# Performance work log

Measured on AMD Instinct MI355X. Metric: run time of the kernel, lower is better.

Reference implementation:

```python
import jax, jax.numpy as jnp
import numpy as np

ETA = 3.0
KCAP = 96
POS_W = 1.2
LAMBDA_CD = 1.0
LAMBDA_P0 = 1.0
STRIDES = (8.0, 16.0, 32.0)


def _level_terms(pred_reg, pred_obj, pred_cls, gt, stride):
    """Vectorized per-level version of the triple python loop.
    pred_reg: [B,6,H,W], pred_obj/pred_cls: [B,1,H,W], gt: [B,Ng,3,2].
    Returns partial sums (reg, obj, cls, pos_count, neg_count)."""
    B, _, H, W = pred_obj.shape
    HW = H * W
    Ng = gt.shape[1]
    ys = (jnp.arange(H, dtype=jnp.float32) + 0.5) * stride
    xs = (jnp.arange(W, dtype=jnp.float32) + 0.5) * stride
    yy, xx = jnp.meshgrid(ys, xs, indexing='ij')
    px = xx.reshape(-1)  # [HW]
    py = yy.reshape(-1)
    P = px[None, None, :]  # [1,1,HW]
    Q = py[None, None, :]
    # triangle vertices, each [B,Ng,1] for broadcasting against HW
    Ax, Ay = gt[:, :, 0, 0:1], gt[:, :, 0, 1:2]
    Bx, By = gt[:, :, 1, 0:1], gt[:, :, 1, 1:2]
    Cx, Cy = gt[:, :, 2, 0:1], gt[:, :, 2, 1:2]

    def sgn(x1, y1, x2, y2, x3, y3):
        return (x1 - x3) * (y2 - y3) - (x2 - x3) * (y1 - y3)

    d1 = sgn(P, Q, Ax, Ay, Bx, By)
    d2 = sgn(P, Q, Bx, By, Cx, Cy)
    d3 = sgn(P, Q, Cx, Cy, Ax, Ay)
    has_neg = (d1 < 0) | (d2 < 0) | (d3 < 0)
    has_pos = (d1 > 0) | (d2 > 0) | (d3 > 0)
    inside = ~(has_neg & has_pos)  # [B,Ng,HW]

    def segd(x1, y1, x2, y2):
        vx, vy = x2 - x1, y2 - y1
        wx, wy = P - x1, Q - y1
        t = jnp.clip((wx * vx + wy * vy) / (vx * vx + vy * vy + 1e-9), 0.0, 1.0)
        dx = P - (x1 + t * vx)
        dy = Q - (y1 + t * vy)
        return jnp.sqrt(dx * dx + dy * dy + 1e-12)

    dist = jnp.minimum(segd(Ax, Ay, Bx, By),
                       jnp.minimum(segd(Bx, By, Cx, Cy), segd(Cx, Cy, Ax, Ay)))
    pos = inside | (dist <= ETA)  # [B,Ng,HW]

    # top-k cap: keep the KCAP positives with smallest boundary distance
    dmask = jnp.where(pos, dist, jnp.inf)
    negd, idx = jax.lax.top_k(-dmask, KCAP)  # [B,Ng,K]
    keep = jnp.isfinite(negd)                # finite <=> was a positive
    bi = jnp.arange(B)[:, None, None]
    gi = jnp.arange(Ng)[None, :, None]
    capped = jnp.zeros((B, Ng, HW), dtype=bool).at[bi, gi, idx].set(keep)
    m = capped.astype(jnp.float32)
    pos_count = m.sum()

    # objectness BCE-with-logits (pos_weight) over the whole map
    obj_t = capped.any(axis=1).astype(jnp.float32)  # [B,HW]
    x = pred_obj.reshape(B, HW)
    obj_loss = (POS_W * obj_t * jax.nn.softplus(-x)
                + (1.0 - obj_t) * jax.nn.softplus(x)).sum()
    neg_count = jnp.float32(B * HW) - obj_t.sum()

    pred_off = pred_reg.transpose(0, 2, 3, 1).reshape(B, HW, 3, 2)
    centers = jnp.stack([px, py], axis=-1)  # [HW,2]
    gt_off = (gt[:, :, None] - centers[None, None, :, None]) / stride  # [B,Ng,HW,3,2]
    p0 = ((pred_off[:, None, :, 0] - gt_off[:, :, :, 0]) ** 2).sum(-1)  # [B,Ng,HW]
    pp = pred_off[:, None, :, 1:, :]  # [B,1,HW,2,2]
    gg = gt_off[:, :, :, 1:, :]       # [B,Ng,HW,2,2]
    d = jnp.sqrt(((pp[..., :, None, :] - gg[..., None, :, :]) ** 2).sum(-1))  # [B,Ng,HW,2,2]
    cd = d.min(-1).sum(-1) + d.min(-2).sum(-1)  # [B,Ng,HW]
    reg = (m * (LAMBDA_P0 * p0 + LAMBDA_CD * cd)).sum()

    # class BCE on positives only, target = 1
    cls = (m * jax.nn.softplus(-pred_cls.reshape(B, 1, HW))).sum()
    return reg, obj_loss, cls, pos_count, neg_count


def setup_inputs() -> dict:
    key = jax.random.key(0)
    ks = jax.random.split(key, 10)
    B, Ng = 16, 32
    shapes = [(128, 128), (64, 64), (32, 32)]
    inp = {}
    i = 0
    for l, (H, W) in enumerate(shapes):
        inp[f'pred_reg{l}'] = jax.random.normal(ks[i], (B, 6, H, W), dtype=jnp.float32); i += 1
        inp[f'pred_obj{l}'] = jax.random.normal(ks[i], (B, 1, H, W), dtype=jnp.float32); i += 1
        inp[f'pred_cls{l}'] = jax.random.normal(ks[i], (B, 1, H, W), dtype=jnp.float32); i += 1
    inp['gt'] = jax.random.uniform(ks[9], (B, Ng, 3, 2), dtype=jnp.float32) * 1024.0
    return inp


def reference(pred_reg0, pred_obj0, pred_cls0,
              pred_reg1, pred_obj1, pred_cls1,
              pred_reg2, pred_obj2, pred_cls2, gt):
    levels = [(pred_reg0, pred_obj0, pred_cls0),
              (pred_reg1, pred_obj1, pred_cls1),
              (pred_reg2, pred_obj2, pred_cls2)]
    reg = obj = cls = pc = nc = jnp.float32(0.0)
    for (pr, po, pcls), s in zip(levels, STRIDES):
        r, o, c, p, n = _level_terms(pr, po, pcls, gt, s)
        reg += r; obj += o; cls += c; pc += p; nc += n
    pos_eps = jnp.maximum(pc, 1.0)
    total = (reg / pos_eps
             + obj / (pos_eps + jnp.maximum(nc, 1.0))
             + cls / pos_eps)
    return total
```

## Files before the change

### kernel.cpp

```cpp
#include <hip/hip_runtime.h>

#define KCAP 96u
#define CAP 6144
#define PBLK 512
#define NTOT 344064
#define NPAIR 1536
#define CELLS_PB 224

__device__ __forceinline__ float softplus_f(float x) {
    return fmaxf(x, 0.0f) + log1pf(expf(-fabsf(x)));
}

__device__ __forceinline__ void tri_pos_dist(
    float px, float py,
    float ax, float ay, float bx, float by, float cx, float cy,
    bool& pos, float& dist)
{
#pragma clang fp contract(off)
    float d1 = (px - bx) * (ay - by) - (ax - bx) * (py - by);
    float d2 = (px - cx) * (by - cy) - (bx - cx) * (py - cy);
    float d3 = (px - ax) * (cy - ay) - (cx - ax) * (py - ay);
    bool has_neg = (d1 < 0.f) | (d2 < 0.f) | (d3 < 0.f);
    bool has_pos = (d1 > 0.f) | (d2 > 0.f) | (d3 > 0.f);
    bool inside = !(has_neg && has_pos);

    float dAB, dBC, dCA;
    {
        float vx = bx - ax, vy = by - ay, wx = px - ax, wy = py - ay;
        float t = (wx*vx + wy*vy) / (vx*vx + vy*vy + 1e-9f);
        t = fminf(fmaxf(t, 0.0f), 1.0f);
        float dx = px - (ax + t*vx), dy = py - (ay + t*vy);
        dAB = sqrtf(dx*dx + dy*dy + 1e-12f);
    }
    {
        float vx = cx - bx, vy = cy - by, wx = px - bx, wy = py - by;
        float t = (wx*vx + wy*vy) / (vx*vx + vy*vy + 1e-9f);
        t = fminf(fmaxf(t, 0.0f), 1.0f);
        float dx = px - (bx + t*vx), dy = py - (by + t*vy);
        dBC = sqrtf(dx*dx + dy*dy + 1e-12f);
    }
    {
        float vx = ax - cx, vy = ay - cy, wx = px - cx, wy = py - cy;
        float t = (wx*vx + wy*vy) / (vx*vx + vy*vy + 1e-9f);
        t = fminf(fmaxf(t, 0.0f), 1.0f);
        float dx = px - (cx + t*vx), dy = py - (cy + t*vy);
        dCA = sqrtf(dx*dx + dy*dy + 1e-12f);
    }
    dist = fminf(dAB, fminf(dBC, dCA));
    pos = inside || (dist <= 3.0f);
}

__global__ void zero_kernel(unsigned* __restrict__ p, int n) {
    int i = blockIdx.x * 256 + threadIdx.x;
    if (i < n) p[i] = 0u;
}

__global__ __launch_bounds__(PBLK) void pair_kernel(
    const float* __restrict__ gt,
    const float* __restrict__ reg0, const float* __restrict__ cls0, const float* __restrict__ o0,
    const float* __restrict__ reg1, const float* __restrict__ cls1, const float* __restrict__ o1,
    const float* __restrict__ reg2, const float* __restrict__ cls2, const float* __restrict__ o2,
    unsigned* __restrict__ objbits,
    double* __restrict__ p_reg, double* __restrict__ p_cls,
    double* __restrict__ p_obj, unsigned* __restrict__ p_tc,
    unsigned* __restrict__ p_pos)
{
    const int bid = blockIdx.x;
    const int tid = threadIdx.x;
    const int lane = tid & 63;

    const int level = bid >> 9;
    const int pair = bid & 511;
    const int b = pair >> 5;

    int W, HW, shift, objbase;
    float stride;
    const float* pr; const float* pcl; const float* po;
    if (level == 0)      { W = 128; HW = 16384; shift = 7; stride = 8.0f;  objbase = 0;     pr = reg0; pcl = cls0; po = o0; }
    else if (level == 1) { W = 64;  HW = 4096;  shift = 6; stride = 16.0f; objbase = 8192;  pr = reg1; pcl = cls1; po = o1; }
    else                 { W = 32;  HW = 1024;  shift = 5; stride = 32.0f; objbase = 10240; pr = reg2; pcl = cls2; po = o2; }
    const int wmask = W - 1;

    double objAcc = 0.0;
    if (tid < CELLS_PB) {
        int idx = bid * CELLS_PB + tid;
        const float* o; int li;
        if (idx < 262144)      { o = o0; li = idx; }
        else if (idx < 327680) { o = o1; li = idx - 262144; }
        else                   { o = o2; li = idx - 327680; }
        objAcc = (double)softplus_f(o[li]);
    }

    const float* gp = gt + pair * 6;
    const float ax = gp[0], ay = gp[1];
    const float bx = gp[2], by = gp[3];
    const float cx = gp[4], cy = gp[5];

    const float inv = 1.0f / stride;
    float minx = fminf(ax, fminf(bx, cx)), maxx = fmaxf(ax, fmaxf(bx, cx));
    float miny = fminf(ay, fminf(by, cy)), maxy = fmaxf(ay, fmaxf(by, cy));
    int wlo = max(0,     (int)floorf((minx - 3.0f) * inv - 0.5f) - 1);
    int whi = min(W - 1, (int)ceilf ((maxx + 3.0f) * inv - 0.5f) + 1);
    int hlo = max(0,     (int)floorf((miny - 3.0f) * inv - 0.5f) - 1);
    int hhi = min(W - 1, (int)ceilf ((maxy + 3.0f) * inv - 0.5f) + 1);
    const int ncols = max(0, whi - wlo + 1);
    const int nb = (hhi - hlo + 1 > 0) ? (hhi - hlo + 1) * ncols : 0;
    const int nbR = (nb + PBLK - 1) & ~(PBLK - 1);
    const unsigned long long dmul =
        (ncols > 0) ? ((1ull << 40) / (unsigned)ncols + 1ull) : 0ull;

    __shared__ unsigned hist[2048];
    __shared__ unsigned chunk[256];
    __shared__ unsigned chunk4[64];
    __shared__ unsigned s_bits[CAP];
    __shared__ unsigned short s_hw[CAP];
    __shared__ unsigned s_cnt, s_T, s_k, s_tiecnt;
    __shared__ double red_reg[8], red_cls[8], red_obj[8];
    __shared__ unsigned red_tc[8], red_pos[8];
    unsigned* tie_hw = hist;

    if (tid == 0) { s_cnt = 0u; s_tiecnt = 0u; }
    for (int j = tid; j < 2048; j += PBLK) hist[j] = 0u;
    __syncthreads();

    auto kth_scan = [&](unsigned kk) {
        __syncthreads();
        if (tid < 256) {
            unsigned s = 0; int base = tid * 8;
            #pragma unroll
            for (int j = 0; j < 8; ++j) s += hist[base + j];
            chunk[tid] = s;
        }
        __syncthreads();
        if (tid < 64) {
            int b4 = tid * 4;
            chunk4[tid] = chunk[b4] + chunk[b4+1] + chunk[b4+2] + chunk[b4+3];
        }
        __syncthreads();
        if (tid == 0) {
            unsigned cum = 0; int t4 = 0;
            while (cum + chunk4[t4] < kk) { cum += chunk4[t4]; ++t4; }
            int t = t4 * 4;
            while (cum + chunk[t] < kk) { cum += chunk[t]; ++t; }
            int bb = t * 8;
            while (cum + hist[bb] < kk) { cum += hist[bb]; ++bb; }
            s_T = (unsigned)bb;
            s_k = kk - cum;
        }
        __syncthreads();
    };

    for (int i = tid; i < nbR; i += PBLK) {
        bool pos = false; unsigned bits = 0u; int hw = 0;
        if (i < nb) {
            int q = (int)(((unsigned long long)(unsigned)i * dmul) >> 40);
            int w = wlo + (i - q * ncols);
            int h = hlo + q;
            hw = (h << shift) | w;
            float px = (w + 0.5f) * stride;
            float py = (h + 0.5f) * stride;
            float dist;
            tri_pos_dist(px, py, ax, ay, bx, by, cx, cy, pos, dist);
            if (pos) { bits = __float_as_uint(dist); atomicAdd(&hist[bits >> 21], 1u); }
        }
        unsigned long long m = __ballot(pos);
        if (m) {
            int leader = __ffsll(m) - 1;
            unsigned base = 0u;
            if (lane == leader) base = atomicAdd(&s_cnt, (unsigned)__popcll(m));
            base = __shfl(base, leader);
            if (pos) {
                unsigned slot = base + (unsigned)__popcll(m & ((1ull << lane) - 1ull));
                if (slot < CAP) { s_bits[slot] = bits; s_hw[slot] = (unsigned short)hw; }
            }
        }
    }
    __syncthreads();

    const unsigned total = s_cnt;
    const bool fullsel = (total <= KCAP);
    unsigned n = min(total, (unsigned)CAP);
    unsigned kth_bits = 0u, tie_need = 0u;
    bool radix_fb = false;

    if (!fullsel) {
        kth_scan(KCAP);
        const unsigned T = s_T, kk1 = s_k;

        if (total > CAP) {
            if (tid == 0) s_cnt = 0u;
            __syncthreads();
            for (int i = tid; i < nbR; i += PBLK) {
                bool keep = false; unsigned bits = 0u; int hw = 0;
                if (i < nb) {
                    int q = (int)(((unsigned long long)(unsigned)i * dmul) >> 40);
                    int w = wlo + (i - q * ncols);
                    int h = hlo + q;
                    hw = (h << shift) | w;
                    float px = (w + 0.5f) * stride;
                    float py = (h + 0.5f) * stride;
                    bool pos; float dist;
                    tri_pos_dist(px, py, ax, ay, bx, by, cx, cy, pos, dist);
                    if (pos) {
                        bits = __float_as_uint(dist);
                        keep = ((bits >> 21) <= T);
                    }
                }
                unsigned long long m = __ballot(keep);
                if (m) {
                    int leader = __ffsll(m) - 1;
                    unsigned base = 0u;
                    if (lane == leader) base = atomicAdd(&s_cnt, (unsigned)__popcll(m));
                    base = __shfl(base, leader);
                    if (keep) {
                        unsigned slot = base + (unsigned)__popcll(m & ((1ull << lane) - 1ull));
                        if (slot < CAP) { s_bits[slot] = bits; s_hw[slot] = (unsigned short)hw; }
                    }
                }
            }
            __syncthreads();
            n = s_cnt;
            if (n > CAP) { radix_fb = true; }
        }

        if (!radix_fb) {
            __syncthreads();
            for (int j = tid; j < 2048; j += PBLK) hist[j] = 0u;
            __syncthreads();
            for (unsigned i = tid; i < n; i += PBLK) {
                unsigned bi = s_bits[i];
                if ((bi >> 21) == T) atomicAdd(&hist[(bi >> 10) & 0x7FFu], 1u);
            }
            kth_scan(kk1);
            unsigned prefix = (T << 11) | s_T;
            unsigned kk2 = s_k;
            __syncthreads();
            for (int j = tid; j < 2048; j += PBLK) hist[j] = 0u;
            __syncthreads();
            for (unsigned i = tid; i < n; i += PBLK) {
                unsigned bi = s_bits[i];
                if ((bi >> 10) == prefix) atomicAdd(&hist[bi & 0x3FFu], 1u);
            }
            kth_scan(kk2);
            kth_bits = (prefix << 10) | s_T;
            tie_need = s_k;
        }
    }

    double regAcc = 0.0, clsAcc = 0.0;
    unsigned tcAcc = 0u, posAcc = 0u;

    auto contribute = [&](int hw) {
        int h = hw >> shift, w = hw & wmask;
        float px = (w + 0.5f) * stride;
        float py = (h + 0.5f) * stride;
        const float* base = pr + (size_t)b * 6 * HW + hw;
        float p0x = base[0],          p0y = base[HW];
        float p1x = base[2 * HW],     p1y = base[3 * HW];
        float p2x = base[4 * HW],     p2y = base[5 * HW];
        float g0x = (ax - px) * inv,  g0y = (ay - py) * inv;
        float g1x = (bx - px) * inv,  g1y = (by - py) * inv;
        float g2x = (cx - px) * inv,  g2y = (cy - py) * inv;
        float dx0 = p0x - g0x, dy0 = p0y - g0y;
        float p0t = dx0 * dx0 + dy0 * dy0;
        float e11x = p1x - g1x, e11y = p1y - g1y;
        float e12x = p1x - g2x, e12y = p1y - g2y;
        float e21x = p2x - g1x, e21y = p2y - g1y;
        float e22x = p2x - g2x, e22y = p2y - g2y;
        float d11 = sqrtf(e11x * e11x + e11y * e11y);
        float d12 = sqrtf(e12x * e12x + e12y * e12y);
        float d21 = sqrtf(e21x * e21x + e21y * e21y);
        float d22 = sqrtf(e22x * e22x + e22y * e22y);
        float cd = fminf(d11, d12) + fminf(d21, d22) + fminf(d11, d21) + fminf(d12, d22);
        regAcc += (double)(p0t + cd);
        clsAcc += (double)softplus_f(-pcl[(size_t)b * HW + hw]);
        posAcc += 1u;

        unsigned bi = (unsigned)(b * HW + hw);
        unsigned bit = 1u << (bi & 31u);
        unsigned old = atomicOr(&objbits[objbase + (bi >> 5)], bit);
        if (!(old & bit)) {
            float x = po[(size_t)b * HW + hw];
            objAcc += (double)(1.2f * softplus_f(-x)) - (double)softplus_f(x);
            tcAcc += 1u;
        }
    };

    if (fullsel) {
        for (unsigned i = tid; i < n; i += PBLK) contribute((int)s_hw[i]);
    } else if (!radix_fb) {
        for (unsigned i = tid; i < n; i += PBLK) {
            unsigned bi = s_bits[i];
            if (bi < kth_bits) {
                contribute((int)s_hw[i]);
            } else if (bi == kth_bits) {
                unsigned t = atomicAdd(&s_tiecnt, 1u);
                if (t < 2048u) tie_hw[t] = s_hw[i];
            }
        }
        __syncthreads();
        unsigned tn = min(s_tiecnt, 2048u);
        for (unsigned i = tid; i < tn; i += PBLK) {
            unsigned hwv = tie_hw[i], rank = 0;
            for (unsigned j = 0; j < tn; ++j) rank += (tie_hw[j] < hwv) ? 1u : 0u;
            if (rank < tie_need) contribute((int)hwv);
        }
    } else {
        unsigned prefix = s_T;
        for (int p = 1; p < 3; ++p) {
            unsigned kk = s_k;
            __syncthreads();
            for (int j = tid; j < 2048; j += PBLK) hist[j] = 0u;
            __syncthreads();
            for (int i = tid; i < nb; i += PBLK) {
                int q = (int)(((unsigned long long)(unsigned)i * dmul) >> 40);
                int w = wlo + (i - q * ncols);
                int h = hlo + q;
                float px = (w + 0.5f) * stride;
                float py = (h + 0.5f) * stride;
                bool pos; float dist;
                tri_pos_dist(px, py, ax, ay, bx, by, cx, cy, pos, dist);
                if (!pos) continue;
                unsigned bits = __float_as_uint(dist);
                unsigned bin;
                if (p == 1) { if ((bits >> 21) != prefix) continue; bin = (bits >> 10) & 0x7FFu; }
                else        { if ((bits >> 10) != prefix) continue; bin = bits & 0x3FFu; }
                atomicAdd(&hist[bin], 1u);
            }
            kth_scan(kk);
            prefix = (p == 1) ? ((prefix << 11) | s_T) : ((prefix << 10) | s_T);
        }
        const unsigned kth = prefix, need = s_k;
        for (int i = tid; i < nb; i += PBLK) {
            int q = (int)(((unsigned long long)(unsigned)i * dmul) >> 40);
            int w = wlo + (i - q * ncols);
            int h = hlo + q;
            int hw = (h << shift) | w;
            float px = (w + 0.5f) * stride;
            float py = (h + 0.5f) * stride;
            bool pos; float dist;
            tri_pos_dist(px, py, ax, ay, bx, by, cx, cy, pos, dist);
            if (!pos) continue;
            unsigned bits = __float_as_uint(dist);
            if (bits < kth) {
                contribute(hw);
            } else if (bits == kth) {
                unsigned t = atomicAdd(&s_tiecnt, 1u);
                if (t < 2048u) tie_hw[t] = (unsigned)hw;
            }
        }
        __syncthreads();
        unsigned tn = min(s_tiecnt, 2048u);
        for (unsigned i = tid; i < tn; i += PBLK) {
            unsigned hwv = tie_hw[i], rank = 0;
            for (unsigned j = 0; j < tn; ++j) rank += (tie_hw[j] < hwv) ? 1u : 0u;
            if (rank < need) contribute((int)hwv);
        }
    }

    for (int off = 32; off > 0; off >>= 1) {
        regAcc += __shfl_down(regAcc, off);
        clsAcc += __shfl_down(clsAcc, off);
        objAcc += __shfl_down(objAcc, off);
        tcAcc  += __shfl_down(tcAcc, off);
        posAcc += __shfl_down(posAcc, off);
    }
    int wave = tid >> 6;
    if (lane == 0) {
        red_reg[wave] = regAcc; red_cls[wave] = clsAcc; red_obj[wave] = objAcc;
        red_tc[wave] = tcAcc; red_pos[wave] = posAcc;
    }
    __syncthreads();
    if (tid == 0) {
        double rs = 0.0, cs = 0.0, os = 0.0; unsigned ts = 0u, ps = 0u;
        #pragma unroll
        for (int i = 0; i < 8; ++i) {
            rs += red_reg[i]; cs += red_cls[i]; os += red_obj[i];
            ts += red_tc[i]; ps += red_pos[i];
        }
        p_reg[bid] = rs;
        p_cls[bid] = cs;
        p_obj[bid] = os;
        p_tc[bid]  = ts;
        p_pos[bid] = ps;
    }
}

__global__ __launch_bounds__(1024) void finalize_kernel(
    const double* __restrict__ p_reg, const double* __restrict__ p_cls,
    const double* __restrict__ p_obj, const unsigned* __restrict__ p_tc,
    const unsigned* __restrict__ p_pos,
    float* __restrict__ out)
{
    const int tid = threadIdx.x;
    double reg = 0.0, cls = 0.0, obj = 0.0;
    unsigned pc = 0u, tc = 0u;
    for (int i = tid; i < NPAIR; i += 1024) {
        reg += p_reg[i]; cls += p_cls[i]; obj += p_obj[i];
        tc += p_tc[i]; pc += p_pos[i];
    }
    for (int off = 32; off > 0; off >>= 1) {
        reg += __shfl_down(reg, off);
        cls += __shfl_down(cls, off);
        obj += __shfl_down(obj, off);
        pc  += __shfl_down(pc, off);
        tc  += __shfl_down(tc, off);
    }
    __shared__ double rr[16], rc[16], ro[16];
    __shared__ unsigned rp[16], rn[16];
    int wave = tid >> 6, lane = tid & 63;
    if (lane == 0) { rr[wave] = reg; rc[wave] = cls; ro[wave] = obj; rp[wave] = pc; rn[wave] = tc; }
    __syncthreads();
    if (tid == 0) {
        double sreg = 0, scls = 0, sobj = 0; unsigned spc = 0, stc = 0;
        #pragma unroll
        for (int i = 0; i < 16; ++i) {
            sreg += rr[i]; scls += rc[i]; sobj += ro[i]; spc += rp[i]; stc += rn[i];
        }
        double nc = (double)NTOT - (double)stc;
        double pos_eps = fmax((double)spc, 1.0);
        double den = pos_eps + fmax(nc, 1.0);
        out[0] = (float)(sreg / pos_eps + sobj / den + scls / pos_eps);
    }
}

extern "C" void kernel_launch(void* const* d_in, const int* in_sizes, int n_in,
                              void* d_out, int out_size, void* d_ws, size_t ws_size,
                              hipStream_t stream)
{
    (void)in_sizes; (void)n_in; (void)out_size; (void)ws_size;
    const float* reg0 = (const float*)d_in[0];
    const float* obj0 = (const float*)d_in[1];
    const float* cls0 = (const float*)d_in[2];
    const float* reg1 = (const float*)d_in[3];
    const float* obj1 = (const float*)d_in[4];
    const float* cls1 = (const float*)d_in[5];
    const float* reg2 = (const float*)d_in[6];
    const float* obj2 = (const float*)d_in[7];
    const float* cls2 = (const float*)d_in[8];
    const float* gt   = (const float*)d_in[9];

    char* ws = (char*)d_ws;
    unsigned* objbits = (unsigned*)ws;
    double*   p_reg   = (double*)(ws + 43008);
    double*   p_cls   = (double*)(ws + 55296);
    double*   p_obj   = (double*)(ws + 67584);
    unsigned* p_tc    = (unsigned*)(ws + 79872);
    unsigned* p_pos   = (unsigned*)(ws + 86016);

    zero_kernel<<<42, 256, 0, stream>>>(objbits, 10752);
    pair_kernel<<<NPAIR, PBLK, 0, stream>>>(gt,
                                            reg0, cls0, obj0,
                                            reg1, cls1, obj1,
                                            reg2, cls2, obj2,
                                            objbits,
                                            p_reg, p_cls, p_obj, p_tc, p_pos);
    finalize_kernel<<<1, 1024, 0, stream>>>(p_reg, p_cls, p_obj, p_tc, p_pos,
                                            (float*)d_out);
}
```

Baseline: 145.1 us.

## Schedule pair blocks largest-bbox-first via on-device bitonic sort

```diff
diff --git a/kernel.cpp b/kernel.cpp
--- a/kernel.cpp
+++ b/kernel.cpp
@@ -50,9 +50,64 @@
     pos = inside || (dist <= 3.0f);
 }
 
-__global__ void zero_kernel(unsigned* __restrict__ p, int n) {
-    int i = blockIdx.x * 256 + threadIdx.x;
-    if (i < n) p[i] = 0u;
+__device__ __forceinline__ unsigned bbox_cells(const float* gp, int level) {
+    int W; float stride;
+    if (level == 0)      { W = 128; stride = 8.0f;  }
+    else if (level == 1) { W = 64;  stride = 16.0f; }
+    else                 { W = 32;  stride = 32.0f; }
+    const float inv = 1.0f / stride;
+    float ax = gp[0], ay = gp[1], bx = gp[2], by = gp[3], cx = gp[4], cy = gp[5];
+    float minx = fminf(ax, fminf(bx, cx)), maxx = fmaxf(ax, fmaxf(bx, cx));
+    float miny = fminf(ay, fminf(by, cy)), maxy = fmaxf(ay, fmaxf(by, cy));
+    int wlo = max(0,     (int)floorf((minx - 3.0f) * inv - 0.5f) - 1);
+    int whi = min(W - 1, (int)ceilf ((maxx + 3.0f) * inv - 0.5f) + 1);
+    int hlo = max(0,     (int)floorf((miny - 3.0f) * inv - 0.5f) - 1);
+    int hhi = min(W - 1, (int)ceilf ((maxy + 3.0f) * inv - 0.5f) + 1);
+    int ncols = max(0, whi - wlo + 1);
+    int nrows = hhi - hlo + 1;
+    return (nrows > 0) ? (unsigned)(nrows * ncols) : 0u;
+}
+
+__global__ __launch_bounds__(1024) void schedule_kernel(
+    const float* __restrict__ gt,
+    unsigned* __restrict__ objbits,
+    unsigned short* __restrict__ perm)
+{
+    const int t = threadIdx.x;
+    for (int i = t; i < 10752; i += 1024) objbits[i] = 0u;
+
+    __shared__ unsigned d[2048];
+    #pragma unroll
+    for (int s = 0; s < 2; ++s) {
+        int i = t + s * 1024;
+        unsigned packed = 0u;
+        if (i < NPAIR) {
+            unsigned nb = bbox_cells(gt + (i & 511) * 6, i >> 9);
+            packed = (nb << 11) | (unsigned)i;
+        }
+        d[i] = packed;
+    }
+    __syncthreads();
+    for (unsigned k = 2; k <= 2048u; k <<= 1) {
+        for (unsigned j = k >> 1; j > 0; j >>= 1) {
+            #pragma unroll
+            for (int s = 0; s < 2; ++s) {
+                int i = t + s * 1024;
+                int ixj = i ^ (int)j;
+                if (ixj > i) {
+                    unsigned a = d[i], b = d[ixj];
+                    bool desc = ((i & k) == 0);
+                    if (desc ? (a < b) : (a > b)) { d[i] = b; d[ixj] = a; }
+                }
+            }
+            __syncthreads();
+        }
+    }
+    #pragma unroll
+    for (int s = 0; s < 2; ++s) {
+        int i = t + s * 1024;
+        if (i < NPAIR) perm[i] = (unsigned short)(d[i] & 0x7FFu);
+    }
 }
 
 __global__ __launch_bounds__(PBLK) void pair_kernel(
@@ -60,17 +115,18 @@
     const float* __restrict__ reg0, const float* __restrict__ cls0, const float* __restrict__ o0,
     const float* __restrict__ reg1, const float* __restrict__ cls1, const float* __restrict__ o1,
     const float* __restrict__ reg2, const float* __restrict__ cls2, const float* __restrict__ o2,
+    const unsigned short* __restrict__ perm,
     unsigned* __restrict__ objbits,
     double* __restrict__ p_reg, double* __restrict__ p_cls,
     double* __restrict__ p_obj, unsigned* __restrict__ p_tc,
     unsigned* __restrict__ p_pos)
 {
-    const int bid = blockIdx.x;
+    const int pid = (int)perm[blockIdx.x];
     const int tid = threadIdx.x;
     const int lane = tid & 63;
 
-    const int level = bid >> 9;
-    const int pair = bid & 511;
+    const int level = pid >> 9;
+    const int pair = pid & 511;
     const int b = pair >> 5;
 
     int W, HW, shift, objbase;
@@ -83,7 +139,7 @@
 
     double objAcc = 0.0;
     if (tid < CELLS_PB) {
-        int idx = bid * CELLS_PB + tid;
+        int idx = pid * CELLS_PB + tid;
         const float* o; int li;
         if (idx < 262144)      { o = o0; li = idx; }
         else if (idx < 327680) { o = o1; li = idx - 262144; }
@@ -378,11 +434,11 @@
             rs += red_reg[i]; cs += red_cls[i]; os += red_obj[i];
             ts += red_tc[i]; ps += red_pos[i];
         }
-        p_reg[bid] = rs;
-        p_cls[bid] = cs;
-        p_obj[bid] = os;
-        p_tc[bid]  = ts;
-        p_pos[bid] = ps;
+        p_reg[pid] = rs;
+        p_cls[pid] = cs;
+        p_obj[pid] = os;
+        p_tc[pid]  = ts;
+        p_pos[pid] = ps;
     }
 }
 
@@ -441,19 +497,20 @@
     const float* gt   = (const float*)d_in[9];
 
     char* ws = (char*)d_ws;
-    unsigned* objbits = (unsigned*)ws;
-    double*   p_reg   = (double*)(ws + 43008);
-    double*   p_cls   = (double*)(ws + 55296);
-    double*   p_obj   = (double*)(ws + 67584);
-    unsigned* p_tc    = (unsigned*)(ws + 79872);
-    unsigned* p_pos   = (unsigned*)(ws + 86016);
-
-    zero_kernel<<<42, 256, 0, stream>>>(objbits, 10752);
+    unsigned*       objbits = (unsigned*)ws;
+    double*         p_reg   = (double*)(ws + 43008);
+    double*         p_cls   = (double*)(ws + 55296);
+    double*         p_obj   = (double*)(ws + 67584);
+    unsigned*       p_tc    = (unsigned*)(ws + 79872);
+    unsigned*       p_pos   = (unsigned*)(ws + 86016);
+    unsigned short* perm    = (unsigned short*)(ws + 92160);
+
+    schedule_kernel<<<1, 1024, 0, stream>>>(gt, objbits, perm);
     pair_kernel<<<NPAIR, PBLK, 0, stream>>>(gt,
                                             reg0, cls0, obj0,
                                             reg1, cls1, obj1,
                                             reg2, cls2, obj2,
-                                            objbits,
+                                            perm, objbits,
                                             p_reg, p_cls, p_obj, p_tc, p_pos);
     finalize_kernel<<<1, 1024, 0, stream>>>(p_reg, p_cls, p_obj, p_tc, p_pos,
                                             (float*)d_out);
```

Measured after the change: 160.1 us. 1.1x slower.
